# Kernel tuning notes

Hardware: AMD Instinct MI355X
Metric: run time of the kernel (lower is better)

The kernel has to match this reference:

```python
import jax, jax.numpy as jnp
import numpy as np

N_NODES = 50000
N_EDGES = 800000
D_IN = 96
D_HID = 96
D_OUT = 4


def _glorot(key, shape):
    lim = float(np.sqrt(6.0 / (shape[0] + shape[1])))
    return jax.random.uniform(key, shape, jnp.float32, -lim, lim)


def setup_inputs() -> dict:
    key = jax.random.key(0)
    ks = jax.random.split(key, 8)
    x = jax.random.normal(ks[0], (N_NODES, D_IN), jnp.float32)
    edge_index = jax.random.randint(ks[1], (2, N_EDGES), 0, N_NODES, jnp.int64)
    return {
        'x': x,
        'edge_index': edge_index,
        'W0': _glorot(ks[2], (D_IN, D_HID)), 'b0': jnp.zeros((D_HID,), jnp.float32),
        'W1': _glorot(ks[3], (D_HID, D_HID)), 'b1': jnp.zeros((D_HID,), jnp.float32),
        'W2': _glorot(ks[4], (D_HID, D_HID)), 'b2': jnp.zeros((D_HID,), jnp.float32),
        'Wfc': _glorot(ks[5], (D_HID, D_OUT)), 'bfc': jnp.zeros((D_OUT,), jnp.float32),
    }


def _gcn_conv(x, src, dst, W, b, n):
    # GCNConv: linear transform, add self-loops, symmetric degree norm, scatter-add.
    h = x @ W                                   # [N, D]
    loops = jnp.arange(n, dtype=src.dtype)
    s = jnp.concatenate([src, loops])           # [E+N]
    d = jnp.concatenate([dst, loops])
    deg = jax.ops.segment_sum(jnp.ones_like(d, dtype=h.dtype), d, num_segments=n)
    dinv = jnp.where(deg > 0, jax.lax.rsqrt(deg), 0.0)
    norm = dinv[s] * dinv[d]                    # [E+N]
    msgs = h[s] * norm[:, None]                 # gather + scale
    out = jax.ops.segment_sum(msgs, d, num_segments=n)  # scatter-add
    return out + b


def reference(x, edge_index, W0, b0, W1, b1, W2, b2, Wfc, bfc):
    src, dst = edge_index[0], edge_index[1]
    n = x.shape[0]
    h = jax.nn.relu(_gcn_conv(x, src, dst, W0, b0, n))   # dropout = identity (eval)
    h = jax.nn.relu(_gcn_conv(h, src, dst, W1, b1, n))
    h = jax.nn.relu(_gcn_conv(h, src, dst, W2, b2, n))
    return h @ Wfc + bfc
```

## Files before the change

kernel.cpp:

```cpp
#include <hip/hip_runtime.h>

typedef __bf16 bf16x8 __attribute__((ext_vector_type(8)));
typedef float  f32x4  __attribute__((ext_vector_type(4)));
typedef float  f32x8  __attribute__((ext_vector_type(8)));
typedef unsigned short ushort;
typedef ushort us8 __attribute__((ext_vector_type(8)));

constexpr int N_NODES = 50000;
constexpr int N_EDGES = 800000;
constexpr int SLOTS = 64;
constexpr int GE   = N_EDGES / 256;
constexpr int GMF  = (N_NODES + 63) / 64;
constexpr int WBLK = (3 * 9216) / 256;
constexpr int AGG_NODES = 32;
constexpr int GAGG = (N_NODES + AGG_NODES - 1) / AGG_NODES;

__device__ inline float h16f(ushort u) {
    union { _Float16 h; ushort u; } cv; cv.u = u; return (float)cv.h;
}
__device__ inline ushort f16b(float f) {
    union { _Float16 h; ushort u; } cv; cv.h = (_Float16)f; return cv.u;
}
__device__ inline ushort bf16b(float f) {
    union { __bf16 b; ushort u; } cv; cv.b = (__bf16)f; return cv.u;
}
__device__ inline f32x8 bf8_to_f32(us8 u) {
    f32x8 r;
#pragma unroll
    for (int i = 0; i < 8; ++i) r[i] = __uint_as_float(((unsigned int)u[i]) << 16);
    return r;
}

__global__ __launch_bounds__(256) void k_count(const int* __restrict__ dst,
                                               int* __restrict__ cnt,
                                               ushort* __restrict__ rank,
                                               const float* __restrict__ W0,
                                               const float* __restrict__ W1,
                                               const float* __restrict__ W2,
                                               ushort* __restrict__ Wt) {
    const int b = blockIdx.x;
    if (b < GE) {
        int e = b * 256 + threadIdx.x;
        rank[e] = (ushort)atomicAdd(&cnt[dst[e]], 1);
    } else {
        int i = (b - GE) * 256 + threadIdx.x;
        int m = i / 9216, li = i - m * 9216;
        const float* W = (m == 0) ? W0 : (m == 1) ? W1 : W2;
        int k = li / 96, c = li - k * 96;
        Wt[m * 9216 + c * 96 + k] = bf16b(W[li]);
    }
}

__device__ __forceinline__ void mfma_store(const ushort* sX, const ushort* sW,
                                           ushort* __restrict__ Y, int rowbase) {
    const int tid = threadIdx.x;
    const int wv = tid >> 6, lane = tid & 63, quad = lane >> 4, l16 = lane & 15;
    f32x4 acc[6];
#pragma unroll
    for (int t = 0; t < 6; ++t) acc[t] = (f32x4){0.f, 0.f, 0.f, 0.f};

    const ushort* ax = sX + (wv * 16 + l16) * 96 + quad * 8;
#pragma unroll
    for (int s = 0; s < 3; ++s) {
        bf16x8 a = *(const bf16x8*)(ax + s * 32);
#pragma unroll
        for (int t = 0; t < 6; ++t) {
            bf16x8 b = *(const bf16x8*)(sW + (t * 16 + l16) * 96 + s * 32 + quad * 8);
            acc[t] = __builtin_amdgcn_mfma_f32_16x16x32_bf16(a, b, acc[t], 0, 0, 0);
        }
    }
    const int r0 = rowbase + wv * 16 + quad * 4;
#pragma unroll
    for (int t = 0; t < 6; ++t) {
#pragma unroll
        for (int g = 0; g < 4; ++g) {
            int r = r0 + g;
            if (r < N_NODES) Y[(size_t)r * 96 + t * 16 + l16] = bf16b(acc[t][g]);
        }
    }
}

__global__ __launch_bounds__(256) void k_fill_gemm1(const int* __restrict__ src,
                                                    const int* __restrict__ dst,
                                                    const int* __restrict__ cnt,
                                                    const ushort* __restrict__ rank,
                                                    unsigned int* __restrict__ csr,
                                                    const float* __restrict__ x,
                                                    const ushort* __restrict__ Wt,
                                                    ushort* __restrict__ H) {
    __shared__ ushort sS[64 * 96 + 96 * 96];
    const int b = blockIdx.x;
    const int tid = threadIdx.x;
    if (b < GMF) {
        ushort* sX = sS;
        ushort* sW = sS + 64 * 96;
        const int rowbase = b * 64;
        for (int i = tid; i < 9216 / 8; i += 256)
            ((uint4*)sW)[i] = ((const uint4*)Wt)[i];
        for (int i = tid; i < 64 * 24; i += 256) {
            int r = i / 24, c4 = i % 24;
            int gr = rowbase + r;
            float4 v = make_float4(0.f, 0.f, 0.f, 0.f);
            if (gr < N_NODES) v = ((const float4*)(x + (size_t)gr * 96))[c4];
            ushort* p = sX + r * 96 + c4 * 4;
            p[0] = bf16b(v.x); p[1] = bf16b(v.y); p[2] = bf16b(v.z); p[3] = bf16b(v.w);
        }
        __syncthreads();
        mfma_store(sX, sW, H, rowbase);
    } else {
        int e = (b - GMF) * 256 + tid;
        int s = src[e], d = dst[e];
        float hs = rsqrtf((float)(cnt[s] + 1));
        unsigned int entry = (unsigned int)(ushort)s | ((unsigned int)f16b(hs) << 16);
        csr[(size_t)d * SLOTS + rank[e]] = entry;
    }
}

__global__ __launch_bounds__(384, 4) void k_agg_gemm(const ushort* __restrict__ A,
                                                     const int* __restrict__ cnt,
                                                     const unsigned int* __restrict__ csr,
                                                     const float* __restrict__ bias,
                                                     const ushort* __restrict__ Wt,
                                                     ushort* __restrict__ Y) {
    __shared__ ushort sS[AGG_NODES * 96 + 96 * 96];
    ushort* sX = sS;
    ushort* sW = sS + AGG_NODES * 96;
    const int tid = threadIdx.x;
    const int rowbase = blockIdx.x * AGG_NODES;

    for (int i = tid; i < 9216 / 8; i += 384)
        ((uint4*)sW)[i] = ((const uint4*)Wt)[i];

    const int g = tid / 12;
    const int c = tid - g * 12;
    const int n = rowbase + g;

    f32x8 acc = (f32x8){0.f, 0.f, 0.f, 0.f, 0.f, 0.f, 0.f, 0.f};
    if (n < N_NODES) {
        const int deg = cnt[n];
        const float dn = rsqrtf((float)(deg + 1));
        us8 a0 = *(const us8*)(A + (size_t)n * 96 + c * 8);

        f32x8 nb = (f32x8){0.f, 0.f, 0.f, 0.f, 0.f, 0.f, 0.f, 0.f};
        const unsigned int* row = csr + (size_t)n * SLOTS;
        int j = 0;
        for (; j + 8 <= deg; j += 8) {
            const uint4 q0 = *(const uint4*)(row + j);
            const uint4 q1 = *(const uint4*)(row + j + 4);
            const us8 u0 = *(const us8*)(A + (size_t)(q0.x & 0xFFFFu) * 96 + c * 8);
            const us8 u1 = *(const us8*)(A + (size_t)(q0.y & 0xFFFFu) * 96 + c * 8);
            const us8 u2 = *(const us8*)(A + (size_t)(q0.z & 0xFFFFu) * 96 + c * 8);
            const us8 u3 = *(const us8*)(A + (size_t)(q0.w & 0xFFFFu) * 96 + c * 8);
            const us8 u4 = *(const us8*)(A + (size_t)(q1.x & 0xFFFFu) * 96 + c * 8);
            const us8 u5 = *(const us8*)(A + (size_t)(q1.y & 0xFFFFu) * 96 + c * 8);
            const us8 u6 = *(const us8*)(A + (size_t)(q1.z & 0xFFFFu) * 96 + c * 8);
            const us8 u7 = *(const us8*)(A + (size_t)(q1.w & 0xFFFFu) * 96 + c * 8);
            nb += bf8_to_f32(u0) * h16f((ushort)(q0.x >> 16));
            nb += bf8_to_f32(u1) * h16f((ushort)(q0.y >> 16));
            nb += bf8_to_f32(u2) * h16f((ushort)(q0.z >> 16));
            nb += bf8_to_f32(u3) * h16f((ushort)(q0.w >> 16));
            nb += bf8_to_f32(u4) * h16f((ushort)(q1.x >> 16));
            nb += bf8_to_f32(u5) * h16f((ushort)(q1.y >> 16));
            nb += bf8_to_f32(u6) * h16f((ushort)(q1.z >> 16));
            nb += bf8_to_f32(u7) * h16f((ushort)(q1.w >> 16));
        }
        for (; j + 4 <= deg; j += 4) {
            const uint4 q = *(const uint4*)(row + j);
            const us8 u0 = *(const us8*)(A + (size_t)(q.x & 0xFFFFu) * 96 + c * 8);
            const us8 u1 = *(const us8*)(A + (size_t)(q.y & 0xFFFFu) * 96 + c * 8);
            const us8 u2 = *(const us8*)(A + (size_t)(q.z & 0xFFFFu) * 96 + c * 8);
            const us8 u3 = *(const us8*)(A + (size_t)(q.w & 0xFFFFu) * 96 + c * 8);
            nb += bf8_to_f32(u0) * h16f((ushort)(q.x >> 16));
            nb += bf8_to_f32(u1) * h16f((ushort)(q.y >> 16));
            nb += bf8_to_f32(u2) * h16f((ushort)(q.z >> 16));
            nb += bf8_to_f32(u3) * h16f((ushort)(q.w >> 16));
        }
        for (; j < deg; ++j) {
            const unsigned int e = row[j];
            const us8 u = *(const us8*)(A + (size_t)(e & 0xFFFFu) * 96 + c * 8);
            nb += bf8_to_f32(u) * h16f((ushort)(e >> 16));
        }
        acc = (nb + bf8_to_f32(a0) * dn) * dn;
#pragma unroll
        for (int f = 0; f < 8; ++f) acc[f] = fmaxf(acc[f] + bias[c * 8 + f], 0.0f);
    }
    {
        us8 o;
#pragma unroll
        for (int f = 0; f < 8; ++f) o[f] = bf16b(acc[f]);
        *(us8*)(sX + g * 96 + c * 8) = o;
    }
    __syncthreads();

    const int wv = tid >> 6;
    const int lane = tid & 63, quad = lane >> 4, l16 = lane & 15;
    const int t0 = 2 * wv;
    const int rg = t0 / 6;
    const int ct0 = t0 - rg * 6;

    f32x4 acc0 = (f32x4){0.f, 0.f, 0.f, 0.f};
    f32x4 acc1 = (f32x4){0.f, 0.f, 0.f, 0.f};
    const ushort* ax = sX + (rg * 16 + l16) * 96 + quad * 8;
#pragma unroll
    for (int s = 0; s < 3; ++s) {
        bf16x8 a = *(const bf16x8*)(ax + s * 32);
        bf16x8 b0 = *(const bf16x8*)(sW + (ct0 * 16 + l16) * 96 + s * 32 + quad * 8);
        bf16x8 b1 = *(const bf16x8*)(sW + ((ct0 + 1) * 16 + l16) * 96 + s * 32 + quad * 8);
        acc0 = __builtin_amdgcn_mfma_f32_16x16x32_bf16(a, b0, acc0, 0, 0, 0);
        acc1 = __builtin_amdgcn_mfma_f32_16x16x32_bf16(a, b1, acc1, 0, 0, 0);
    }
    const int r0 = rowbase + rg * 16 + quad * 4;
#pragma unroll
    for (int gg = 0; gg < 4; ++gg) {
        int r = r0 + gg;
        if (r < N_NODES) {
            Y[(size_t)r * 96 + ct0 * 16 + l16]       = bf16b(acc0[gg]);
            Y[(size_t)r * 96 + (ct0 + 1) * 16 + l16] = bf16b(acc1[gg]);
        }
    }
}

__global__ __launch_bounds__(192) void k_agg_fc(const ushort* __restrict__ A,
                                                const int* __restrict__ cnt,
                                                const unsigned int* __restrict__ csr,
                                                const float* __restrict__ bias,
                                                float* __restrict__ out4,
                                                const float* __restrict__ Wfc,
                                                const float* __restrict__ bfc) {
    __shared__ float sWfc[384];
    __shared__ float red[16][12][4];
    const int tid = threadIdx.x;
    for (int i = tid; i < 384; i += 192) sWfc[i] = Wfc[i];
    __syncthreads();
    const int g = tid / 12, c = tid % 12;
    const int n = blockIdx.x * 16 + g;

    const int deg = cnt[n];
    const float dn = rsqrtf((float)(deg + 1));
    us8 a0 = *(const us8*)(A + (size_t)n * 96 + c * 8);

    f32x8 nb = (f32x8){0.f, 0.f, 0.f, 0.f, 0.f, 0.f, 0.f, 0.f};
    const unsigned int* row = csr + (size_t)n * SLOTS;
    int j = 0;
    for (; j + 8 <= deg; j += 8) {
        const uint4 q0 = *(const uint4*)(row + j);
        const uint4 q1 = *(const uint4*)(row + j + 4);
        const us8 u0 = *(const us8*)(A + (size_t)(q0.x & 0xFFFFu) * 96 + c * 8);
        const us8 u1 = *(const us8*)(A + (size_t)(q0.y & 0xFFFFu) * 96 + c * 8);
        const us8 u2 = *(const us8*)(A + (size_t)(q0.z & 0xFFFFu) * 96 + c * 8);
        const us8 u3 = *(const us8*)(A + (size_t)(q0.w & 0xFFFFu) * 96 + c * 8);
        const us8 u4 = *(const us8*)(A + (size_t)(q1.x & 0xFFFFu) * 96 + c * 8);
        const us8 u5 = *(const us8*)(A + (size_t)(q1.y & 0xFFFFu) * 96 + c * 8);
        const us8 u6 = *(const us8*)(A + (size_t)(q1.z & 0xFFFFu) * 96 + c * 8);
        const us8 u7 = *(const us8*)(A + (size_t)(q1.w & 0xFFFFu) * 96 + c * 8);
        nb += bf8_to_f32(u0) * h16f((ushort)(q0.x >> 16));
        nb += bf8_to_f32(u1) * h16f((ushort)(q0.y >> 16));
        nb += bf8_to_f32(u2) * h16f((ushort)(q0.z >> 16));
        nb += bf8_to_f32(u3) * h16f((ushort)(q0.w >> 16));
        nb += bf8_to_f32(u4) * h16f((ushort)(q1.x >> 16));
        nb += bf8_to_f32(u5) * h16f((ushort)(q1.y >> 16));
        nb += bf8_to_f32(u6) * h16f((ushort)(q1.z >> 16));
        nb += bf8_to_f32(u7) * h16f((ushort)(q1.w >> 16));
    }
    for (; j + 4 <= deg; j += 4) {
        const uint4 q = *(const uint4*)(row + j);
        const us8 u0 = *(const us8*)(A + (size_t)(q.x & 0xFFFFu) * 96 + c * 8);
        const us8 u1 = *(const us8*)(A + (size_t)(q.y & 0xFFFFu) * 96 + c * 8);
        const us8 u2 = *(const us8*)(A + (size_t)(q.z & 0xFFFFu) * 96 + c * 8);
        const us8 u3 = *(const us8*)(A + (size_t)(q.w & 0xFFFFu) * 96 + c * 8);
        nb += bf8_to_f32(u0) * h16f((ushort)(q.x >> 16));
        nb += bf8_to_f32(u1) * h16f((ushort)(q.y >> 16));
        nb += bf8_to_f32(u2) * h16f((ushort)(q.z >> 16));
        nb += bf8_to_f32(u3) * h16f((ushort)(q.w >> 16));
    }
    for (; j < deg; ++j) {
        const unsigned int e = row[j];
        const us8 u = *(const us8*)(A + (size_t)(e & 0xFFFFu) * 96 + c * 8);
        nb += bf8_to_f32(u) * h16f((ushort)(e >> 16));
    }
    f32x8 acc = (nb + bf8_to_f32(a0) * dn) * dn;
#pragma unroll
    for (int f = 0; f < 8; ++f) acc[f] = fmaxf(acc[f] + bias[c * 8 + f], 0.0f);

    float p0 = 0.f, p1 = 0.f, p2 = 0.f, p3 = 0.f;
#pragma unroll
    for (int f = 0; f < 8; ++f) {
        const float* wr = sWfc + (c * 8 + f) * 4;
        p0 += acc[f] * wr[0];
        p1 += acc[f] * wr[1];
        p2 += acc[f] * wr[2];
        p3 += acc[f] * wr[3];
    }
    red[g][c][0] = p0; red[g][c][1] = p1; red[g][c][2] = p2; red[g][c][3] = p3;
    __syncthreads();
    if (tid < 64) {
        const int gg = tid >> 2, jj = tid & 3;
        float s = bfc[jj];
#pragma unroll
        for (int cc = 0; cc < 12; ++cc) s += red[gg][cc][jj];
        out4[(size_t)(blockIdx.x * 16 + gg) * 4 + jj] = s;
    }
}

extern "C" void kernel_launch(void* const* d_in, const int* in_sizes, int n_in,
                              void* d_out, int out_size, void* d_ws, size_t ws_size,
                              hipStream_t stream) {
    const float* x   = (const float*)d_in[0];
    const int*   ei  = (const int*)d_in[1];
    const int*   src = ei;
    const int*   dst = ei + N_EDGES;
    const float* W0  = (const float*)d_in[2];
    const float* b0  = (const float*)d_in[3];
    const float* W1  = (const float*)d_in[4];
    const float* b1  = (const float*)d_in[5];
    const float* W2  = (const float*)d_in[6];
    const float* b2  = (const float*)d_in[7];
    const float* Wfc = (const float*)d_in[8];
    const float* bfc = (const float*)d_in[9];
    float* out = (float*)d_out;

    char* w = (char*)d_ws;
    unsigned int* csr = (unsigned int*)w;  w += ((size_t)N_NODES * SLOTS * 4 + 15) & ~15ULL;
    int*    cnt  = (int*)w;                w += ((size_t)N_NODES * 4 + 15) & ~15ULL;
    ushort* rank = (ushort*)w;             w += ((size_t)N_EDGES * 2 + 15) & ~15ULL;
    ushort* Wt   = (ushort*)w;             w += ((size_t)3 * 9216 * 2 + 15) & ~15ULL;
    ushort* H    = (ushort*)w;             w += ((size_t)N_NODES * 96 * 2 + 15) & ~15ULL;
    ushort* G    = (ushort*)w;

    (void)hipMemsetAsync(cnt, 0, (size_t)N_NODES * 4, stream);
    hipLaunchKernelGGL(k_count, dim3(GE + WBLK), dim3(256), 0, stream,
                       dst, cnt, rank, W0, W1, W2, Wt);
    hipLaunchKernelGGL(k_fill_gemm1, dim3(GMF + GE), dim3(256), 0, stream,
                       src, dst, cnt, rank, csr, x, Wt, H);
    hipLaunchKernelGGL(k_agg_gemm, dim3(GAGG), dim3(384), 0, stream,
                       H, cnt, csr, b0, Wt + 9216, G);
    hipLaunchKernelGGL(k_agg_gemm, dim3(GAGG), dim3(384), 0, stream,
                       G, cnt, csr, b1, Wt + 2 * 9216, H);
    hipLaunchKernelGGL(k_agg_fc, dim3(N_NODES / 16), dim3(192), 0, stream,
                       H, cnt, csr, b2, out, Wfc, bfc);
}
```

Baseline: 224.4 us.

## Fold source-degree normalization into GEMM epilogue and shrink CSR to 16-bit indices

The per-source rsqrt(deg) factor is now applied once per row when each GEMM stores its bf16 output, instead of being packed into each CSR entry as an fp16 scale. CSR entries become plain 16-bit source indices, which halves adjacency storage and traffic and removes the per-edge scale multiply in all aggregation kernels. Nontemporal load/store hints are also added on streaming edge, rank, x and CSR accesses. The change shifts where rounding to bf16 happens, which slightly alters numerics.

```diff
diff --git a/kernel.cpp b/kernel.cpp
--- a/kernel.cpp
+++ b/kernel.cpp
@@ -5,6 +5,7 @@
 typedef float  f32x8  __attribute__((ext_vector_type(8)));
 typedef unsigned short ushort;
 typedef ushort us8 __attribute__((ext_vector_type(8)));
+typedef ushort us4 __attribute__((ext_vector_type(4)));
 
 constexpr int N_NODES = 50000;
 constexpr int N_EDGES = 800000;
@@ -15,12 +16,6 @@
 constexpr int AGG_NODES = 32;
 constexpr int GAGG = (N_NODES + AGG_NODES - 1) / AGG_NODES;
 
-__device__ inline float h16f(ushort u) {
-    union { _Float16 h; ushort u; } cv; cv.u = u; return (float)cv.h;
-}
-__device__ inline ushort f16b(float f) {
-    union { _Float16 h; ushort u; } cv; cv.h = (_Float16)f; return cv.u;
-}
 __device__ inline ushort bf16b(float f) {
     union { __bf16 b; ushort u; } cv; cv.b = (__bf16)f; return cv.u;
 }
@@ -41,7 +36,9 @@
     const int b = blockIdx.x;
     if (b < GE) {
         int e = b * 256 + threadIdx.x;
-        rank[e] = (ushort)atomicAdd(&cnt[dst[e]], 1);
+        int d = __builtin_nontemporal_load(&dst[e]);
+        ushort r = (ushort)atomicAdd(&cnt[d], 1);
+        __builtin_nontemporal_store(r, &rank[e]);
     } else {
         int i = (b - GE) * 256 + threadIdx.x;
         int m = i / 9216, li = i - m * 9216;
@@ -52,6 +49,7 @@
 }
 
 __device__ __forceinline__ void mfma_store(const ushort* sX, const ushort* sW,
+                                           const int* __restrict__ cnt,
                                            ushort* __restrict__ Y, int rowbase) {
     const int tid = threadIdx.x;
     const int wv = tid >> 6, lane = tid & 63, quad = lane >> 4, l16 = lane & 15;
@@ -71,11 +69,13 @@
     }
     const int r0 = rowbase + wv * 16 + quad * 4;
 #pragma unroll
-    for (int t = 0; t < 6; ++t) {
-#pragma unroll
-        for (int g = 0; g < 4; ++g) {
-            int r = r0 + g;
-            if (r < N_NODES) Y[(size_t)r * 96 + t * 16 + l16] = bf16b(acc[t][g]);
+    for (int g = 0; g < 4; ++g) {
+        int r = r0 + g;
+        if (r < N_NODES) {
+            float dv = rsqrtf((float)(cnt[r] + 1));
+#pragma unroll
+            for (int t = 0; t < 6; ++t)
+                Y[(size_t)r * 96 + t * 16 + l16] = bf16b(acc[t][g] * dv);
         }
     }
 }
@@ -84,7 +84,7 @@
                                                     const int* __restrict__ dst,
                                                     const int* __restrict__ cnt,
                                                     const ushort* __restrict__ rank,
-                                                    unsigned int* __restrict__ csr,
+                                                    ushort* __restrict__ csr,
                                                     const float* __restrict__ x,
                                                     const ushort* __restrict__ Wt,
                                                     ushort* __restrict__ H) {
@@ -100,25 +100,25 @@
         for (int i = tid; i < 64 * 24; i += 256) {
             int r = i / 24, c4 = i % 24;
             int gr = rowbase + r;
-            float4 v = make_float4(0.f, 0.f, 0.f, 0.f);
-            if (gr < N_NODES) v = ((const float4*)(x + (size_t)gr * 96))[c4];
+            f32x4 v = (f32x4){0.f, 0.f, 0.f, 0.f};
+            if (gr < N_NODES) v = __builtin_nontemporal_load((const f32x4*)(x + (size_t)gr * 96) + c4);
             ushort* p = sX + r * 96 + c4 * 4;
-            p[0] = bf16b(v.x); p[1] = bf16b(v.y); p[2] = bf16b(v.z); p[3] = bf16b(v.w);
+            p[0] = bf16b(v[0]); p[1] = bf16b(v[1]); p[2] = bf16b(v[2]); p[3] = bf16b(v[3]);
         }
         __syncthreads();
-        mfma_store(sX, sW, H, rowbase);
+        mfma_store(sX, sW, cnt, H, rowbase);
     } else {
         int e = (b - GMF) * 256 + tid;
-        int s = src[e], d = dst[e];
-        float hs = rsqrtf((float)(cnt[s] + 1));
-        unsigned int entry = (unsigned int)(ushort)s | ((unsigned int)f16b(hs) << 16);
-        csr[(size_t)d * SLOTS + rank[e]] = entry;
+        int s = __builtin_nontemporal_load(&src[e]);
+        int d = __builtin_nontemporal_load(&dst[e]);
+        ushort rk = __builtin_nontemporal_load(&rank[e]);
+        __builtin_nontemporal_store((ushort)s, &csr[(size_t)d * SLOTS + rk]);
     }
 }
 
 __global__ __launch_bounds__(384, 4) void k_agg_gemm(const ushort* __restrict__ A,
                                                      const int* __restrict__ cnt,
-                                                     const unsigned int* __restrict__ csr,
+                                                     const ushort* __restrict__ csr,
                                                      const float* __restrict__ bias,
                                                      const ushort* __restrict__ Wt,
                                                      ushort* __restrict__ Y) {
@@ -142,45 +142,44 @@
         us8 a0 = *(const us8*)(A + (size_t)n * 96 + c * 8);
 
         f32x8 nb = (f32x8){0.f, 0.f, 0.f, 0.f, 0.f, 0.f, 0.f, 0.f};
-        const unsigned int* row = csr + (size_t)n * SLOTS;
+        const ushort* row = csr + (size_t)n * SLOTS;
         int j = 0;
         for (; j + 8 <= deg; j += 8) {
-            const uint4 q0 = *(const uint4*)(row + j);
-            const uint4 q1 = *(const uint4*)(row + j + 4);
-            const us8 u0 = *(const us8*)(A + (size_t)(q0.x & 0xFFFFu) * 96 + c * 8);
-            const us8 u1 = *(const us8*)(A + (size_t)(q0.y & 0xFFFFu) * 96 + c * 8);
-            const us8 u2 = *(const us8*)(A + (size_t)(q0.z & 0xFFFFu) * 96 + c * 8);
-            const us8 u3 = *(const us8*)(A + (size_t)(q0.w & 0xFFFFu) * 96 + c * 8);
-            const us8 u4 = *(const us8*)(A + (size_t)(q1.x & 0xFFFFu) * 96 + c * 8);
-            const us8 u5 = *(const us8*)(A + (size_t)(q1.y & 0xFFFFu) * 96 + c * 8);
-            const us8 u6 = *(const us8*)(A + (size_t)(q1.z & 0xFFFFu) * 96 + c * 8);
-            const us8 u7 = *(const us8*)(A + (size_t)(q1.w & 0xFFFFu) * 96 + c * 8);
-            nb += bf8_to_f32(u0) * h16f((ushort)(q0.x >> 16));
-            nb += bf8_to_f32(u1) * h16f((ushort)(q0.y >> 16));
-            nb += bf8_to_f32(u2) * h16f((ushort)(q0.z >> 16));
-            nb += bf8_to_f32(u3) * h16f((ushort)(q0.w >> 16));
-            nb += bf8_to_f32(u4) * h16f((ushort)(q1.x >> 16));
-            nb += bf8_to_f32(u5) * h16f((ushort)(q1.y >> 16));
-            nb += bf8_to_f32(u6) * h16f((ushort)(q1.z >> 16));
-            nb += bf8_to_f32(u7) * h16f((ushort)(q1.w >> 16));
+            const us8 q = __builtin_nontemporal_load((const us8*)(row + j));
+            const us8 u0 = *(const us8*)(A + (size_t)q[0] * 96 + c * 8);
+            const us8 u1 = *(const us8*)(A + (size_t)q[1] * 96 + c * 8);
+            const us8 u2 = *(const us8*)(A + (size_t)q[2] * 96 + c * 8);
+            const us8 u3 = *(const us8*)(A + (size_t)q[3] * 96 + c * 8);
+            const us8 u4 = *(const us8*)(A + (size_t)q[4] * 96 + c * 8);
+            const us8 u5 = *(const us8*)(A + (size_t)q[5] * 96 + c * 8);
+            const us8 u6 = *(const us8*)(A + (size_t)q[6] * 96 + c * 8);
+            const us8 u7 = *(const us8*)(A + (size_t)q[7] * 96 + c * 8);
+            nb += bf8_to_f32(u0);
+            nb += bf8_to_f32(u1);
+            nb += bf8_to_f32(u2);
+            nb += bf8_to_f32(u3);
+            nb += bf8_to_f32(u4);
+            nb += bf8_to_f32(u5);
+            nb += bf8_to_f32(u6);
+            nb += bf8_to_f32(u7);
         }
         for (; j + 4 <= deg; j += 4) {
-            const uint4 q = *(const uint4*)(row + j);
-            const us8 u0 = *(const us8*)(A + (size_t)(q.x & 0xFFFFu) * 96 + c * 8);
-            const us8 u1 = *(const us8*)(A + (size_t)(q.y & 0xFFFFu) * 96 + c * 8);
-            const us8 u2 = *(const us8*)(A + (size_t)(q.z & 0xFFFFu) * 96 + c * 8);
-            const us8 u3 = *(const us8*)(A + (size_t)(q.w & 0xFFFFu) * 96 + c * 8);
-            nb += bf8_to_f32(u0) * h16f((ushort)(q.x >> 16));
-            nb += bf8_to_f32(u1) * h16f((ushort)(q.y >> 16));
-            nb += bf8_to_f32(u2) * h16f((ushort)(q.z >> 16));
-            nb += bf8_to_f32(u3) * h16f((ushort)(q.w >> 16));
+            const us4 q = __builtin_nontemporal_load((const us4*)(row + j));
+            const us8 u0 = *(const us8*)(A + (size_t)q[0] * 96 + c * 8);
+            const us8 u1 = *(const us8*)(A + (size_t)q[1] * 96 + c * 8);
+            const us8 u2 = *(const us8*)(A + (size_t)q[2] * 96 + c * 8);
+            const us8 u3 = *(const us8*)(A + (size_t)q[3] * 96 + c * 8);
+            nb += bf8_to_f32(u0);
+            nb += bf8_to_f32(u1);
+            nb += bf8_to_f32(u2);
+            nb += bf8_to_f32(u3);
         }
         for (; j < deg; ++j) {
-            const unsigned int e = row[j];
-            const us8 u = *(const us8*)(A + (size_t)(e & 0xFFFFu) * 96 + c * 8);
-            nb += bf8_to_f32(u) * h16f((ushort)(e >> 16));
-        }
-        acc = (nb + bf8_to_f32(a0) * dn) * dn;
+            const int s = __builtin_nontemporal_load(row + j);
+            const us8 u = *(const us8*)(A + (size_t)s * 96 + c * 8);
+            nb += bf8_to_f32(u);
+        }
+        acc = (nb + bf8_to_f32(a0)) * dn;
 #pragma unroll
         for (int f = 0; f < 8; ++f) acc[f] = fmaxf(acc[f] + bias[c * 8 + f], 0.0f);
     }
@@ -214,15 +213,16 @@
     for (int gg = 0; gg < 4; ++gg) {
         int r = r0 + gg;
         if (r < N_NODES) {
-            Y[(size_t)r * 96 + ct0 * 16 + l16]       = bf16b(acc0[gg]);
-            Y[(size_t)r * 96 + (ct0 + 1) * 16 + l16] = bf16b(acc1[gg]);
+            float dv = rsqrtf((float)(cnt[r] + 1));
+            Y[(size_t)r * 96 + ct0 * 16 + l16]       = bf16b(acc0[gg] * dv);
+            Y[(size_t)r * 96 + (ct0 + 1) * 16 + l16] = bf16b(acc1[gg] * dv);
         }
     }
 }
 
 __global__ __launch_bounds__(192) void k_agg_fc(const ushort* __restrict__ A,
                                                 const int* __restrict__ cnt,
-                                                const unsigned int* __restrict__ csr,
+                                                const ushort* __restrict__ csr,
                                                 const float* __restrict__ bias,
                                                 float* __restrict__ out4,
                                                 const float* __restrict__ Wfc,
@@ -240,45 +240,44 @@
     us8 a0 = *(const us8*)(A + (size_t)n * 96 + c * 8);
 
     f32x8 nb = (f32x8){0.f, 0.f, 0.f, 0.f, 0.f, 0.f, 0.f, 0.f};
-    const unsigned int* row = csr + (size_t)n * SLOTS;
+    const ushort* row = csr + (size_t)n * SLOTS;
     int j = 0;
     for (; j + 8 <= deg; j += 8) {
-        const uint4 q0 = *(const uint4*)(row + j);
-        const uint4 q1 = *(const uint4*)(row + j + 4);
-        const us8 u0 = *(const us8*)(A + (size_t)(q0.x & 0xFFFFu) * 96 + c * 8);
-        const us8 u1 = *(const us8*)(A + (size_t)(q0.y & 0xFFFFu) * 96 + c * 8);
-        const us8 u2 = *(const us8*)(A + (size_t)(q0.z & 0xFFFFu) * 96 + c * 8);
-        const us8 u3 = *(const us8*)(A + (size_t)(q0.w & 0xFFFFu) * 96 + c * 8);
-        const us8 u4 = *(const us8*)(A + (size_t)(q1.x & 0xFFFFu) * 96 + c * 8);
-        const us8 u5 = *(const us8*)(A + (size_t)(q1.y & 0xFFFFu) * 96 + c * 8);
-        const us8 u6 = *(const us8*)(A + (size_t)(q1.z & 0xFFFFu) * 96 + c * 8);
-        const us8 u7 = *(const us8*)(A + (size_t)(q1.w & 0xFFFFu) * 96 + c * 8);
-        nb += bf8_to_f32(u0) * h16f((ushort)(q0.x >> 16));
-        nb += bf8_to_f32(u1) * h16f((ushort)(q0.y >> 16));
-        nb += bf8_to_f32(u2) * h16f((ushort)(q0.z >> 16));
-        nb += bf8_to_f32(u3) * h16f((ushort)(q0.w >> 16));
-        nb += bf8_to_f32(u4) * h16f((ushort)(q1.x >> 16));
-        nb += bf8_to_f32(u5) * h16f((ushort)(q1.y >> 16));
-        nb += bf8_to_f32(u6) * h16f((ushort)(q1.z >> 16));
-        nb += bf8_to_f32(u7) * h16f((ushort)(q1.w >> 16));
+        const us8 q = __builtin_nontemporal_load((const us8*)(row + j));
+        const us8 u0 = *(const us8*)(A + (size_t)q[0] * 96 + c * 8);
+        const us8 u1 = *(const us8*)(A + (size_t)q[1] * 96 + c * 8);
+        const us8 u2 = *(const us8*)(A + (size_t)q[2] * 96 + c * 8);
+        const us8 u3 = *(const us8*)(A + (size_t)q[3] * 96 + c * 8);
+        const us8 u4 = *(const us8*)(A + (size_t)q[4] * 96 + c * 8);
+        const us8 u5 = *(const us8*)(A + (size_t)q[5] * 96 + c * 8);
+        const us8 u6 = *(const us8*)(A + (size_t)q[6] * 96 + c * 8);
+        const us8 u7 = *(const us8*)(A + (size_t)q[7] * 96 + c * 8);
+        nb += bf8_to_f32(u0);
+        nb += bf8_to_f32(u1);
+        nb += bf8_to_f32(u2);
+        nb += bf8_to_f32(u3);
+        nb += bf8_to_f32(u4);
+        nb += bf8_to_f32(u5);
+        nb += bf8_to_f32(u6);
+        nb += bf8_to_f32(u7);
     }
     for (; j + 4 <= deg; j += 4) {
-        const uint4 q = *(const uint4*)(row + j);
-        const us8 u0 = *(const us8*)(A + (size_t)(q.x & 0xFFFFu) * 96 + c * 8);
-        const us8 u1 = *(const us8*)(A + (size_t)(q.y & 0xFFFFu) * 96 + c * 8);
-        const us8 u2 = *(const us8*)(A + (size_t)(q.z & 0xFFFFu) * 96 + c * 8);
-        const us8 u3 = *(const us8*)(A + (size_t)(q.w & 0xFFFFu) * 96 + c * 8);
-        nb += bf8_to_f32(u0) * h16f((ushort)(q.x >> 16));
-        nb += bf8_to_f32(u1) * h16f((ushort)(q.y >> 16));
-        nb += bf8_to_f32(u2) * h16f((ushort)(q.z >> 16));
-        nb += bf8_to_f32(u3) * h16f((ushort)(q.w >> 16));
+        const us4 q = __builtin_nontemporal_load((const us4*)(row + j));
+        const us8 u0 = *(const us8*)(A + (size_t)q[0] * 96 + c * 8);
+        const us8 u1 = *(const us8*)(A + (size_t)q[1] * 96 + c * 8);
+        const us8 u2 = *(const us8*)(A + (size_t)q[2] * 96 + c * 8);
+        const us8 u3 = *(const us8*)(A + (size_t)q[3] * 96 + c * 8);
+        nb += bf8_to_f32(u0);
+        nb += bf8_to_f32(u1);
+        nb += bf8_to_f32(u2);
+        nb += bf8_to_f32(u3);
     }
     for (; j < deg; ++j) {
-        const unsigned int e = row[j];
-        const us8 u = *(const us8*)(A + (size_t)(e & 0xFFFFu) * 96 + c * 8);
-        nb += bf8_to_f32(u) * h16f((ushort)(e >> 16));
-    }
-    f32x8 acc = (nb + bf8_to_f32(a0) * dn) * dn;
+        const int s = __builtin_nontemporal_load(row + j);
+        const us8 u = *(const us8*)(A + (size_t)s * 96 + c * 8);
+        nb += bf8_to_f32(u);
+    }
+    f32x8 acc = (nb + bf8_to_f32(a0)) * dn;
 #pragma unroll
     for (int f = 0; f < 8; ++f) acc[f] = fmaxf(acc[f] + bias[c * 8 + f], 0.0f);
 
@@ -320,7 +319,7 @@
     float* out = (float*)d_out;
 
     char* w = (char*)d_ws;
-    unsigned int* csr = (unsigned int*)w;  w += ((size_t)N_NODES * SLOTS * 4 + 15) & ~15ULL;
+    ushort* csr = (ushort*)w;              w += ((size_t)N_NODES * SLOTS * 2 + 15) & ~15ULL;
     int*    cnt  = (int*)w;                w += ((size_t)N_NODES * 4 + 15) & ~15ULL;
     ushort* rank = (ushort*)w;             w += ((size_t)N_EDGES * 2 + 15) & ~15ULL;
     ushort* Wt   = (ushort*)w;             w += ((size_t)3 * 9216 * 2 + 15) & ~15ULL;
```

Measured after the change: 236.1 us. 1.05x slower.

## Replace memset with zero-init kernel and overlap edge counting with first GEMM

Applied to the files above, without the earlier changes.

The hipMemsetAsync of the degree counters becomes a vectorized zeroing pass inside a new init kernel that also transposes the weights. The atomic degree counting moves into the same launch as the first-layer GEMM, and CSR filling becomes its own kernel. The goal is to drop the memset call and overlap the latency-bound atomics with the MFMA work. The launch count stays the same, but the fill pass now runs alone instead of sharing a launch with the GEMM.

```diff
diff --git a/kernel.cpp b/kernel.cpp
--- a/kernel.cpp
+++ b/kernel.cpp
@@ -11,6 +11,7 @@
 constexpr int SLOTS = 64;
 constexpr int GE   = N_EDGES / 256;
 constexpr int GMF  = (N_NODES + 63) / 64;
+constexpr int ZBLK = (12500 + 255) / 256;
 constexpr int WBLK = (3 * 9216) / 256;
 constexpr int AGG_NODES = 32;
 constexpr int GAGG = (N_NODES + AGG_NODES - 1) / AGG_NODES;
@@ -31,19 +32,19 @@
     return r;
 }
 
-__global__ __launch_bounds__(256) void k_count(const int* __restrict__ dst,
-                                               int* __restrict__ cnt,
-                                               ushort* __restrict__ rank,
-                                               const float* __restrict__ W0,
-                                               const float* __restrict__ W1,
-                                               const float* __restrict__ W2,
-                                               ushort* __restrict__ Wt) {
+__global__ __launch_bounds__(256) void k_init(int* __restrict__ cnt,
+                                              const float* __restrict__ W0,
+                                              const float* __restrict__ W1,
+                                              const float* __restrict__ W2,
+                                              ushort* __restrict__ Wt) {
     const int b = blockIdx.x;
-    if (b < GE) {
-        int e = b * 256 + threadIdx.x;
-        rank[e] = (ushort)atomicAdd(&cnt[dst[e]], 1);
+    const int tid = threadIdx.x;
+    if (b < ZBLK) {
+        int i = b * 256 + tid;
+        if (i < 12500)
+            ((uint4*)cnt)[i] = make_uint4(0, 0, 0, 0);
     } else {
-        int i = (b - GE) * 256 + threadIdx.x;
+        int i = (b - ZBLK) * 256 + tid;
         int m = i / 9216, li = i - m * 9216;
         const float* W = (m == 0) ? W0 : (m == 1) ? W1 : W2;
         int k = li / 96, c = li - k * 96;
@@ -80,14 +81,12 @@
     }
 }
 
-__global__ __launch_bounds__(256) void k_fill_gemm1(const int* __restrict__ src,
-                                                    const int* __restrict__ dst,
-                                                    const int* __restrict__ cnt,
-                                                    const ushort* __restrict__ rank,
-                                                    unsigned int* __restrict__ csr,
-                                                    const float* __restrict__ x,
-                                                    const ushort* __restrict__ Wt,
-                                                    ushort* __restrict__ H) {
+__global__ __launch_bounds__(256) void k_count_g1(const int* __restrict__ dst,
+                                                  int* __restrict__ cnt,
+                                                  ushort* __restrict__ rank,
+                                                  const float* __restrict__ x,
+                                                  const ushort* __restrict__ Wt,
+                                                  ushort* __restrict__ H) {
     __shared__ ushort sS[64 * 96 + 96 * 96];
     const int b = blockIdx.x;
     const int tid = threadIdx.x;
@@ -109,11 +108,20 @@
         mfma_store(sX, sW, H, rowbase);
     } else {
         int e = (b - GMF) * 256 + tid;
-        int s = src[e], d = dst[e];
-        float hs = rsqrtf((float)(cnt[s] + 1));
-        unsigned int entry = (unsigned int)(ushort)s | ((unsigned int)f16b(hs) << 16);
-        csr[(size_t)d * SLOTS + rank[e]] = entry;
-    }
+        rank[e] = (ushort)atomicAdd(&cnt[dst[e]], 1);
+    }
+}
+
+__global__ __launch_bounds__(256) void k_fill(const int* __restrict__ src,
+                                              const int* __restrict__ dst,
+                                              const int* __restrict__ cnt,
+                                              const ushort* __restrict__ rank,
+                                              unsigned int* __restrict__ csr) {
+    int e = blockIdx.x * 256 + threadIdx.x;
+    int s = src[e], d = dst[e];
+    float hs = rsqrtf((float)(cnt[s] + 1));
+    unsigned int entry = (unsigned int)(ushort)s | ((unsigned int)f16b(hs) << 16);
+    csr[(size_t)d * SLOTS + rank[e]] = entry;
 }
 
 __global__ __launch_bounds__(384, 4) void k_agg_gemm(const ushort* __restrict__ A,
@@ -327,11 +335,12 @@
     ushort* H    = (ushort*)w;             w += ((size_t)N_NODES * 96 * 2 + 15) & ~15ULL;
     ushort* G    = (ushort*)w;
 
-    (void)hipMemsetAsync(cnt, 0, (size_t)N_NODES * 4, stream);
-    hipLaunchKernelGGL(k_count, dim3(GE + WBLK), dim3(256), 0, stream,
-                       dst, cnt, rank, W0, W1, W2, Wt);
-    hipLaunchKernelGGL(k_fill_gemm1, dim3(GMF + GE), dim3(256), 0, stream,
-                       src, dst, cnt, rank, csr, x, Wt, H);
+    hipLaunchKernelGGL(k_init, dim3(ZBLK + WBLK), dim3(256), 0, stream,
+                       cnt, W0, W1, W2, Wt);
+    hipLaunchKernelGGL(k_count_g1, dim3(GMF + GE), dim3(256), 0, stream,
+                       dst, cnt, rank, x, Wt, H);
+    hipLaunchKernelGGL(k_fill, dim3(GE), dim3(256), 0, stream,
+                       src, dst, cnt, rank, csr);
     hipLaunchKernelGGL(k_agg_gemm, dim3(GAGG), dim3(384), 0, stream,
                        H, cnt, csr, b0, Wt + 9216, G);
     hipLaunchKernelGGL(k_agg_gemm, dim3(GAGG), dim3(384), 0, stream,
```

Result: faster. 217.7 us (median of 2 runs) (-3.0%).
